# Optimization experiments

Measured on AMD Instinct MI355X. Metric: run time of the kernel, lower is better.

Reference implementation:

```python
import jax, jax.numpy as jnp
import numpy as np

B, S, HID = 8, 1024, 1024
NH, HD = 16, 64  # num heads, head dim; NH*HD == HID


def setup_inputs() -> dict:
    key = jax.random.key(0)
    ks = jax.random.split(key, 8)
    sc = 0.02
    return {
        "hidden_states": jax.random.normal(ks[0], (B, S, HID), jnp.float32),
        "attention_mask": jnp.zeros((B, 1, 1, S), jnp.float32),
        "Wq": jax.random.normal(ks[1], (HID, HID), jnp.float32) * sc,
        "bq": jnp.zeros((HID,), jnp.float32),
        "Wk": jax.random.normal(ks[2], (HID, HID), jnp.float32) * sc,
        "bk": jnp.zeros((HID,), jnp.float32),
        "Wv": jax.random.normal(ks[3], (HID, HID), jnp.float32) * sc,
        "bv": jnp.zeros((HID,), jnp.float32),
    }


def reference(hidden_states, attention_mask, Wq, bq, Wk, bk, Wv, bv):
    def split_heads(x):  # [B,S,HID] -> [B,NH,S,HD]
        return x.reshape(B, S, NH, HD).transpose(0, 2, 1, 3)

    q = split_heads(hidden_states @ Wq + bq)
    k = split_heads(hidden_states @ Wk + bk)
    v = split_heads(hidden_states @ Wv + bv)

    # [B,NH,S,S] score matrix, scale, additive mask, softmax
    scores = jnp.einsum("bhqd,bhkd->bhqk", q, k) / jnp.sqrt(jnp.float32(HD))
    scores = scores + attention_mask
    probs = jax.nn.softmax(scores, axis=-1)  # dropout prob = 0.0 -> identity

    ctx = jnp.einsum("bhqk,bhkd->bhqd", probs, v)
    return ctx.transpose(0, 2, 1, 3).reshape(B, S, HID)
```

## Files before the change

### kernel.cpp

```cpp
#include <hip/hip_runtime.h>


typedef __bf16 bf16x8 __attribute__((ext_vector_type(8)));
typedef float f32x4 __attribute__((ext_vector_type(4)));
typedef float f32x16 __attribute__((ext_vector_type(16)));

__device__ __forceinline__ unsigned rne16(float x) {
  unsigned u = __builtin_bit_cast(unsigned, x);
  return (u + 0x7fffu + ((u >> 16) & 1u)) >> 16;
}
__device__ __forceinline__ unsigned packbf(float lo, float hi) {
  return rne16(lo) | (rne16(hi) << 16);
}
__device__ __forceinline__ unsigned packbf_fast(float lo, float hi) {
  unsigned ul = __builtin_bit_cast(unsigned, lo) + 0x8000u;
  unsigned uh = __builtin_bit_cast(unsigned, hi) + 0x8000u;
  return __builtin_amdgcn_perm(uh, ul, 0x07060302u);
}
__device__ __forceinline__ void async16(void* l, const void* g) {
  __builtin_amdgcn_global_load_lds((const __attribute__((address_space(1))) void*)g,
                                   (__attribute__((address_space(3))) void*)l, 16, 0, 0);
}

__global__ __launch_bounds__(256) void k_prep(const float* __restrict__ h,
                                              unsigned short* __restrict__ hbf,
                                              const float* __restrict__ Wq,
                                              const float* __restrict__ Wk,
                                              const float* __restrict__ Wv,
                                              unsigned short* __restrict__ wt) {
  __shared__ float t[32][33];
  int bid = blockIdx.x, tid = threadIdx.x;
  if (bid < 8192) {
    size_t i = (size_t)bid * 256 + tid;
    float4 v = ((const float4*)h)[i];
    uint2 r;
    r.x = packbf(v.x, v.y);
    r.y = packbf(v.z, v.w);
    ((uint2*)hbf)[i] = r;
  } else {
    int id = bid - 8192;
    int which = id >> 10;
    int sub = id & 1023;
    int c0 = (sub & 31) * 32, k0 = (sub >> 5) * 32;
    const float* W = which == 0 ? Wq : (which == 1 ? Wk : Wv);
    int tx = tid & 31, ty = tid >> 5;
#pragma unroll
    for (int i = 0; i < 4; ++i) {
      int r = ty + i * 8;
      t[r][tx] = W[(size_t)(k0 + r) * 1024 + c0 + tx];
    }
    __syncthreads();
#pragma unroll
    for (int i = 0; i < 4; ++i) {
      int r = ty + i * 8;
      wt[((size_t)which * 1024 + c0 + r) * 1024 + k0 + tx] = (unsigned short)rne16(t[tx][r]);
    }
  }
}

__global__ __launch_bounds__(256, 2) void k_gemm(const unsigned short* __restrict__ A,
                                                 const unsigned short* __restrict__ Bm,
                                                 const float* __restrict__ bq,
                                                 const float* __restrict__ bk,
                                                 const float* __restrict__ bv,
                                                 unsigned short* __restrict__ qkv,
                                                 unsigned short* __restrict__ vt) {
  __shared__ __align__(16) char lds[65536];
  const int tid = threadIdx.x;
  const int w = tid >> 6, lane = tid & 63;
  const int wm = w >> 1, wn = w & 1;

  int orig = blockIdx.x;
  int wgid = (orig & 7) * 192 + (orig >> 3);
  int tm = wgid / 24, tn = wgid - tm * 24;
  int m0 = tm * 128, n0 = tn * 128;

  int ro[4], ke[4];
#pragma unroll
  for (int j = 0; j < 4; ++j) {
    int o = j * 4096 + tid * 16;
    int s = o >> 10, w10 = o & 1023;
    int lg = w10 ^ (((w10 >> 9) & 1) << 5);
    ro[j] = ((s >> 1) << 4) + (lg >> 6);
    ke[j] = ((s & 1) << 5) + ((lg & 63) >> 1);
  }
  auto stage = [&](int kt, char* buf) {
    const unsigned short* As = A + (size_t)m0 * 1024 + kt * 64;
    const unsigned short* Bs = Bm + (size_t)n0 * 1024 + kt * 64;
#pragma unroll
    for (int j = 0; j < 4; ++j) {
      async16(buf + j * 4096 + tid * 16, As + (size_t)ro[j] * 1024 + ke[j]);
      async16(buf + 16384 + j * 4096 + tid * 16, Bs + (size_t)ro[j] * 1024 + ke[j]);
    }
  };

  const int lswz = (((lane & 15) << 6) | ((lane >> 4) << 4)) ^ ((lane & 8) << 2);

  f32x4 acc[4][4];
#pragma unroll
  for (int i = 0; i < 4; ++i)
#pragma unroll
    for (int j = 0; j < 4; ++j)
#pragma unroll
      for (int e = 0; e < 4; ++e) acc[i][j][e] = 0.f;

  auto compute = [&](const char* buf) {
    const char* abase = buf + lswz;
    const char* bbase = buf + 16384 + lswz;
#pragma unroll
    for (int ks = 0; ks < 2; ++ks) {
      bf16x8 bF[4];
#pragma unroll
      for (int n = 0; n < 4; ++n)
        bF[n] = *(const bf16x8*)(bbase + ((size_t)((wn * 4 + n) * 2 + ks) << 10));
#pragma unroll
      for (int mt = 0; mt < 4; ++mt) {
        bf16x8 a = *(const bf16x8*)(abase + ((size_t)((wm * 4 + mt) * 2 + ks) << 10));
#pragma unroll
        for (int n = 0; n < 4; ++n)
          acc[mt][n] =
              __builtin_amdgcn_mfma_f32_16x16x32_bf16(a, bF[n], acc[mt][n], 0, 0, 0);
      }
    }
  };

  char* buf0 = lds;
  char* buf1 = lds + 32768;
  stage(0, buf0);
#pragma unroll 1
  for (int kt = 0; kt < 16; kt += 2) {
    __syncthreads();
    stage(kt + 1, buf1);
    compute(buf0);
    __syncthreads();
    if (kt + 2 < 16) stage(kt + 2, buf0);
    compute(buf1);
  }

  const int which = tn >> 3;
  const int ng = n0 & 1023;
  const int b = m0 >> 10;
  const int r = lane & 15, qq = lane >> 4;
  const int sb = (m0 & 1023) + wm * 64 + qq * 4;

  if (which != 2) {
    const float* bp = which == 0 ? bq : bk;
    unsigned short* base = qkv + ((size_t)which << 23) + ((size_t)b << 20);
#pragma unroll
    for (int n = 0; n < 4; ++n) {
      int n_in = ng + wn * 64 + n * 16 + r;
      float bias = bp[n_in];
      unsigned short* dp = base + ((size_t)(n_in >> 6) << 16) + (n_in & 63);
#pragma unroll
      for (int m = 0; m < 4; ++m)
#pragma unroll
        for (int e = 0; e < 4; ++e)
          dp[(size_t)(sb + m * 16 + e) << 6] = (unsigned short)rne16(acc[m][n][e] + bias);
    }
  } else {
    unsigned short* vbase = vt + ((size_t)b << 20);
#pragma unroll
    for (int n = 0; n < 4; ++n) {
      int n_in = ng + wn * 64 + n * 16 + r;
      float bias = bv[n_in];
      unsigned short* dp = vbase + ((size_t)n_in << 10) + sb;
#pragma unroll
      for (int m = 0; m < 4; ++m) {
        uint2 pk;
        pk.x = packbf(acc[m][n][0] + bias, acc[m][n][1] + bias);
        pk.y = packbf(acc[m][n][2] + bias, acc[m][n][3] + bias);
        *(uint2*)(dp + m * 16) = pk;
      }
    }
  }
}

__global__ __launch_bounds__(256, 4) void k_attn(const unsigned short* __restrict__ qg,
                                                 const unsigned short* __restrict__ kg,
                                                 const unsigned short* __restrict__ vtg,
                                                 const float* __restrict__ maskg,
                                                 float* __restrict__ out) {
  __shared__ __align__(16) char lds[36864];
  char* KF = lds;
  char* VF = lds + 16384;
  float* MK = (float*)(lds + 32768);
  int tid = threadIdx.x, w = tid >> 6, lane = tid & 63, l5 = lane & 31, q5 = lane >> 5;
  int idx = blockIdx.x;
  int bi = idx & 7;
  int j = idx >> 3;
  int h = j >> 3, qc = j & 7;
  int bh = bi * 16 + h, s0 = qc * 128;
  const unsigned short* qb = qg + ((size_t)bh << 16);
  const unsigned short* kb = kg + ((size_t)bh << 16);
  const unsigned short* vb = vtg + ((size_t)bh << 16);
  const float LG = 1.4426950408889634f;
  const float C1 = 0.125f * LG;

  {
    float4 mv = *(const float4*)(maskg + (size_t)bi * 1024 + tid * 4);
    mv.x *= LG; mv.y *= LG; mv.z *= LG; mv.w *= LG;
    *(float4*)(MK + tid * 4) = mv;
  }

  bf16x8 qfr[4];
#pragma unroll
  for (int ds = 0; ds < 4; ++ds)
    qfr[ds] = *(const bf16x8*)(qb + (size_t)(s0 + w * 32 + l5) * 64 + ds * 16 + q5 * 8);

  f32x16 O[2];
#pragma unroll
  for (int i = 0; i < 2; ++i)
#pragma unroll
    for (int e = 0; e < 16; ++e) O[i][e] = 0.f;
  float lsum = 0.f;

#pragma unroll 1
  for (int kt = 0; kt < 8; ++kt) {
    int k0 = kt * 128;
    __syncthreads();
#pragma unroll
    for (int t = 0; t < 4; ++t) {
      int f = w * 4 + t, mt = f >> 2, ds = f & 3;
      async16(KF + f * 1024, kb + (size_t)(k0 + mt * 32 + l5) * 64 + ds * 16 + q5 * 8);
    }
#pragma unroll
    for (int t = 0; t < 4; ++t) {
      int f = w * 4 + t, dt = f >> 3, ks = f & 7;
      async16(VF + f * 1024, vb + (size_t)(dt * 32 + l5) * 1024 + k0 + ks * 16 + q5 * 8);
    }
    __syncthreads();

#pragma unroll
    for (int mt = 0; mt < 4; ++mt) {
      f32x16 S;
#pragma unroll
      for (int e = 0; e < 16; ++e) S[e] = 0.f;
#pragma unroll
      for (int ds = 0; ds < 4; ++ds) {
        bf16x8 a = *(const bf16x8*)(KF + (mt * 4 + ds) * 1024 + lane * 16);
        S = __builtin_amdgcn_mfma_f32_32x32x16_bf16(a, qfr[ds], S, 0, 0, 0);
      }
      float p[16];
#pragma unroll
      for (int g4 = 0; g4 < 4; ++g4) {
        float4 mv = *(const float4*)(MK + k0 + mt * 32 + g4 * 8 + q5 * 4);
        p[g4 * 4 + 0] = __builtin_amdgcn_exp2f(S[g4 * 4 + 0] * C1 + mv.x);
        p[g4 * 4 + 1] = __builtin_amdgcn_exp2f(S[g4 * 4 + 1] * C1 + mv.y);
        p[g4 * 4 + 2] = __builtin_amdgcn_exp2f(S[g4 * 4 + 2] * C1 + mv.z);
        p[g4 * 4 + 3] = __builtin_amdgcn_exp2f(S[g4 * 4 + 3] * C1 + mv.w);
      }
      unsigned p2[8];
#pragma unroll
      for (int e = 0; e < 16; ++e) lsum += p[e];
#pragma unroll
      for (int jj = 0; jj < 8; ++jj) p2[jj] = packbf_fast(p[2 * jj], p[2 * jj + 1]);
#pragma unroll
      for (int kh = 0; kh < 2; ++kh) {
        int ks = mt * 2 + kh, gp = kh * 4;
        bf16x8 av0 = *(const bf16x8*)(VF + (0 * 8 + ks) * 1024 + lane * 16);
        bf16x8 av1 = *(const bf16x8*)(VF + (1 * 8 + ks) * 1024 + lane * 16);
        unsigned o0 = p2[gp + 0], o1 = p2[gp + 1];
        unsigned o2 = p2[gp + 2], o3 = p2[gp + 3];
        unsigned t0 = __shfl_xor((int)o0, 32);
        unsigned t1 = __shfl_xor((int)o1, 32);
        unsigned t2 = __shfl_xor((int)o2, 32);
        unsigned t3 = __shfl_xor((int)o3, 32);
        uint4 fu;
        fu.x = q5 ? t2 : o0;
        fu.y = q5 ? t3 : o1;
        fu.z = q5 ? o2 : t0;
        fu.w = q5 ? o3 : t1;
        bf16x8 bfrag = __builtin_bit_cast(bf16x8, fu);
        O[0] = __builtin_amdgcn_mfma_f32_32x32x16_bf16(av0, bfrag, O[0], 0, 0, 0);
        O[1] = __builtin_amdgcn_mfma_f32_32x32x16_bf16(av1, bfrag, O[1], 0, 0, 0);
      }
    }
  }

  __syncthreads();
  float* Ob = (float*)(lds + w * 8192);
  float lt = lsum + __shfl_xor(lsum, 32);
  float rinv = 1.0f / lt;
#pragma unroll
  for (int dt = 0; dt < 2; ++dt)
#pragma unroll
    for (int g4 = 0; g4 < 4; ++g4) {
      float4 val;
      val.x = O[dt][g4 * 4 + 0] * rinv;
      val.y = O[dt][g4 * 4 + 1] * rinv;
      val.z = O[dt][g4 * 4 + 2] * rinv;
      val.w = O[dt][g4 * 4 + 3] * rinv;
      int c = dt * 8 + g4 * 2 + q5;
      *(float4*)(Ob + l5 * 64 + (c ^ (l5 & 15)) * 4) = val;
    }
#pragma unroll
  for (int t = 0; t < 8; ++t) {
    int qr = t * 4 + (lane >> 4), cr = lane & 15;
    float4 vv = *(const float4*)(Ob + qr * 64 + (cr ^ (qr & 15)) * 4);
    int s = s0 + w * 32 + qr;
    *(float4*)(out + (((size_t)(bi * 1024 + s)) << 10) + (h << 6) + (cr << 2)) = vv;
  }
}

extern "C" void kernel_launch(void* const* d_in, const int* in_sizes, int n_in,
                              void* d_out, int out_size, void* d_ws, size_t ws_size,
                              hipStream_t stream) {
  (void)in_sizes; (void)n_in; (void)out_size; (void)ws_size;
  const float* hidden = (const float*)d_in[0];
  const float* mask = (const float*)d_in[1];
  const float* Wq = (const float*)d_in[2];
  const float* bq = (const float*)d_in[3];
  const float* Wk = (const float*)d_in[4];
  const float* bk = (const float*)d_in[5];
  const float* Wv = (const float*)d_in[6];
  const float* bv = (const float*)d_in[7];
  float* out = (float*)d_out;
  char* ws = (char*)d_ws;
  unsigned short* hbf = (unsigned short*)ws;
  unsigned short* wt  = (unsigned short*)(ws + 16777216);
  unsigned short* qkv = (unsigned short*)(ws + 23068672);
  unsigned short* vt  = (unsigned short*)(ws + 56623104);

  k_prep<<<11264, 256, 0, stream>>>(hidden, hbf, Wq, Wk, Wv, wt);
  k_gemm<<<1536, 256, 0, stream>>>(hbf, wt, bq, bk, bv, qkv, vt);
  k_attn<<<1024, 256, 0, stream>>>(qkv, qkv + 8388608, vt, mask, out);
}
```

Before: 211.9 us.

## Load attention K/V fragments directly from global; halve GEMM k-tile for occupancy

Result: slower. 283.0 us (+33.6%).

```diff
diff --git a/kernel.cpp b/kernel.cpp
--- a/kernel.cpp
+++ b/kernel.cpp
@@ -58,14 +58,14 @@
   }
 }
 
-__global__ __launch_bounds__(256, 2) void k_gemm(const unsigned short* __restrict__ A,
+__global__ __launch_bounds__(256, 4) void k_gemm(const unsigned short* __restrict__ A,
                                                  const unsigned short* __restrict__ Bm,
                                                  const float* __restrict__ bq,
                                                  const float* __restrict__ bk,
                                                  const float* __restrict__ bv,
                                                  unsigned short* __restrict__ qkv,
                                                  unsigned short* __restrict__ vt) {
-  __shared__ __align__(16) char lds[65536];
+  __shared__ __align__(16) char lds[32768];
   const int tid = threadIdx.x;
   const int w = tid >> 6, lane = tid & 63;
   const int wm = w >> 1, wn = w & 1;
@@ -75,22 +75,22 @@
   int tm = wgid / 24, tn = wgid - tm * 24;
   int m0 = tm * 128, n0 = tn * 128;
 
-  int ro[4], ke[4];
-#pragma unroll
-  for (int j = 0; j < 4; ++j) {
+  int ro[2], ke[2];
+#pragma unroll
+  for (int j = 0; j < 2; ++j) {
     int o = j * 4096 + tid * 16;
     int s = o >> 10, w10 = o & 1023;
     int lg = w10 ^ (((w10 >> 9) & 1) << 5);
-    ro[j] = ((s >> 1) << 4) + (lg >> 6);
-    ke[j] = ((s & 1) << 5) + ((lg & 63) >> 1);
+    ro[j] = s * 16 + (lg >> 6);
+    ke[j] = (lg & 63) >> 1;
   }
   auto stage = [&](int kt, char* buf) {
-    const unsigned short* As = A + (size_t)m0 * 1024 + kt * 64;
-    const unsigned short* Bs = Bm + (size_t)n0 * 1024 + kt * 64;
-#pragma unroll
-    for (int j = 0; j < 4; ++j) {
+    const unsigned short* As = A + (size_t)m0 * 1024 + kt * 32;
+    const unsigned short* Bs = Bm + (size_t)n0 * 1024 + kt * 32;
+#pragma unroll
+    for (int j = 0; j < 2; ++j) {
       async16(buf + j * 4096 + tid * 16, As + (size_t)ro[j] * 1024 + ke[j]);
-      async16(buf + 16384 + j * 4096 + tid * 16, Bs + (size_t)ro[j] * 1024 + ke[j]);
+      async16(buf + 8192 + j * 4096 + tid * 16, Bs + (size_t)ro[j] * 1024 + ke[j]);
     }
   };
 
@@ -106,34 +106,31 @@
 
   auto compute = [&](const char* buf) {
     const char* abase = buf + lswz;
-    const char* bbase = buf + 16384 + lswz;
-#pragma unroll
-    for (int ks = 0; ks < 2; ++ks) {
-      bf16x8 bF[4];
+    const char* bbase = buf + 8192 + lswz;
+    bf16x8 bF[4];
+#pragma unroll
+    for (int n = 0; n < 4; ++n)
+      bF[n] = *(const bf16x8*)(bbase + ((size_t)(wn * 4 + n) << 10));
+#pragma unroll
+    for (int mt = 0; mt < 4; ++mt) {
+      bf16x8 a = *(const bf16x8*)(abase + ((size_t)(wm * 4 + mt) << 10));
 #pragma unroll
       for (int n = 0; n < 4; ++n)
-        bF[n] = *(const bf16x8*)(bbase + ((size_t)((wn * 4 + n) * 2 + ks) << 10));
-#pragma unroll
-      for (int mt = 0; mt < 4; ++mt) {
-        bf16x8 a = *(const bf16x8*)(abase + ((size_t)((wm * 4 + mt) * 2 + ks) << 10));
-#pragma unroll
-        for (int n = 0; n < 4; ++n)
-          acc[mt][n] =
-              __builtin_amdgcn_mfma_f32_16x16x32_bf16(a, bF[n], acc[mt][n], 0, 0, 0);
-      }
+        acc[mt][n] =
+            __builtin_amdgcn_mfma_f32_16x16x32_bf16(a, bF[n], acc[mt][n], 0, 0, 0);
     }
   };
 
   char* buf0 = lds;
-  char* buf1 = lds + 32768;
+  char* buf1 = lds + 16384;
   stage(0, buf0);
 #pragma unroll 1
-  for (int kt = 0; kt < 16; kt += 2) {
+  for (int kt = 0; kt < 32; kt += 2) {
     __syncthreads();
     stage(kt + 1, buf1);
     compute(buf0);
     __syncthreads();
-    if (kt + 2 < 16) stage(kt + 2, buf0);
+    if (kt + 2 < 32) stage(kt + 2, buf0);
     compute(buf1);
   }
 
@@ -181,9 +178,7 @@
                                                  const float* __restrict__ maskg,
                                                  float* __restrict__ out) {
   __shared__ __align__(16) char lds[36864];
-  char* KF = lds;
-  char* VF = lds + 16384;
-  float* MK = (float*)(lds + 32768);
+  float* MK = (float*)lds;
   int tid = threadIdx.x, w = tid >> 6, lane = tid & 63, l5 = lane & 31, q5 = lane >> 5;
   int idx = blockIdx.x;
   int bi = idx & 7;
@@ -201,11 +196,15 @@
     mv.x *= LG; mv.y *= LG; mv.z *= LG; mv.w *= LG;
     *(float4*)(MK + tid * 4) = mv;
   }
+  __syncthreads();
 
   bf16x8 qfr[4];
 #pragma unroll
   for (int ds = 0; ds < 4; ++ds)
     qfr[ds] = *(const bf16x8*)(qb + (size_t)(s0 + w * 32 + l5) * 64 + ds * 16 + q5 * 8);
+
+  const unsigned short* kp = kb + (size_t)l5 * 64 + q5 * 8;
+  const unsigned short* vp = vb + (size_t)l5 * 1024 + q5 * 8;
 
   f32x16 O[2];
 #pragma unroll
@@ -217,19 +216,6 @@
 #pragma unroll 1
   for (int kt = 0; kt < 8; ++kt) {
     int k0 = kt * 128;
-    __syncthreads();
-#pragma unroll
-    for (int t = 0; t < 4; ++t) {
-      int f = w * 4 + t, mt = f >> 2, ds = f & 3;
-      async16(KF + f * 1024, kb + (size_t)(k0 + mt * 32 + l5) * 64 + ds * 16 + q5 * 8);
-    }
-#pragma unroll
-    for (int t = 0; t < 4; ++t) {
-      int f = w * 4 + t, dt = f >> 3, ks = f & 7;
-      async16(VF + f * 1024, vb + (size_t)(dt * 32 + l5) * 1024 + k0 + ks * 16 + q5 * 8);
-    }
-    __syncthreads();
-
 #pragma unroll
     for (int mt = 0; mt < 4; ++mt) {
       f32x16 S;
@@ -237,7 +223,7 @@
       for (int e = 0; e < 16; ++e) S[e] = 0.f;
 #pragma unroll
       for (int ds = 0; ds < 4; ++ds) {
-        bf16x8 a = *(const bf16x8*)(KF + (mt * 4 + ds) * 1024 + lane * 16);
+        bf16x8 a = *(const bf16x8*)(kp + (size_t)(k0 + mt * 32) * 64 + ds * 16);
         S = __builtin_amdgcn_mfma_f32_32x32x16_bf16(a, qfr[ds], S, 0, 0, 0);
       }
       float p[16];
@@ -257,8 +243,8 @@
 #pragma unroll
       for (int kh = 0; kh < 2; ++kh) {
         int ks = mt * 2 + kh, gp = kh * 4;
-        bf16x8 av0 = *(const bf16x8*)(VF + (0 * 8 + ks) * 1024 + lane * 16);
-        bf16x8 av1 = *(const bf16x8*)(VF + (1 * 8 + ks) * 1024 + lane * 16);
+        bf16x8 av0 = *(const bf16x8*)(vp + k0 + ks * 16);
+        bf16x8 av1 = *(const bf16x8*)(vp + 32 * 1024 + k0 + ks * 16);
         unsigned o0 = p2[gp + 0], o1 = p2[gp + 1];
         unsigned o2 = p2[gp + 2], o3 = p2[gp + 3];
         unsigned t0 = __shfl_xor((int)o0, 32);
@@ -277,8 +263,7 @@
     }
   }
 
-  __syncthreads();
-  float* Ob = (float*)(lds + w * 8192);
+  float* Ob = (float*)(lds + 4096 + w * 8192);
   float lt = lsum + __shfl_xor(lsum, 32);
   float rinv = 1.0f / lt;
 #pragma unroll
```
